# Kernel tuning notes

Hardware: AMD Instinct MI355X
Metric: run time of the kernel (lower is better)

## Reference

```python
import jax, jax.numpy as jnp
import numpy as np

DIM = 1024
NUM_HEADS = 16
NUM_KV_HEADS = 4
HEAD_DIM = DIM // NUM_HEADS  # 64
GROUP = NUM_HEADS // NUM_KV_HEADS  # 4
SCALE = HEAD_DIM ** -0.5


def setup_inputs() -> dict:
    key = jax.random.key(0)
    ks = jax.random.split(key, 6)
    B, N = 2, 2048
    x = jax.random.normal(ks[0], (B, N, DIM), dtype=jnp.float32)
    s = DIM ** -0.5
    Wq = jax.random.normal(ks[1], (DIM, DIM), dtype=jnp.float32) * s
    Wk = jax.random.normal(ks[2], (DIM, NUM_KV_HEADS * HEAD_DIM), dtype=jnp.float32) * s
    Wv = jax.random.normal(ks[3], (DIM, NUM_KV_HEADS * HEAD_DIM), dtype=jnp.float32) * s
    Wo = jax.random.normal(ks[4], (DIM, DIM), dtype=jnp.float32) * s
    bo = jax.random.normal(ks[5], (DIM,), dtype=jnp.float32) * 0.01
    return {"x": x, "Wq": Wq, "Wk": Wk, "Wv": Wv, "Wo": Wo, "bo": bo}


def reference(x, Wq, Wk, Wv, Wo, bo):
    B, N, C = x.shape
    # projections
    q = (x @ Wq).reshape(B, N, NUM_HEADS, HEAD_DIM)          # B N H D
    k = (x @ Wk).reshape(B, N, NUM_KV_HEADS, HEAD_DIM)       # B N Kh D
    v = (x @ Wv).reshape(B, N, NUM_KV_HEADS, HEAD_DIM)
    # group query heads: H = Kh * GROUP; broadcast KV per group (no repeat copy)
    q = q.reshape(B, N, NUM_KV_HEADS, GROUP, HEAD_DIM)
    # scores: B Kh G Nq Nk
    attn = jnp.einsum('bqhgd,bkhd->bhgqk', q, k) * SCALE
    attn = jax.nn.softmax(attn, axis=-1)
    out = jnp.einsum('bhgqk,bkhd->bqhgd', attn, v)           # B N Kh G D
    out = out.reshape(B, N, C)
    return out @ Wo + bo
```

## Files before the change

### kernel.cpp

```cpp
#include <hip/hip_runtime.h>
#include <hip/hip_bf16.h>


typedef unsigned short u16;
typedef short s8 __attribute__((ext_vector_type(8)));
typedef short s4 __attribute__((ext_vector_type(4)));
typedef float f4 __attribute__((ext_vector_type(4)));
typedef u16 u16x8 __attribute__((ext_vector_type(8)));
typedef unsigned int u32x4 __attribute__((ext_vector_type(4)));

__device__ __forceinline__ unsigned pk2(float a, float b) {
  __hip_bfloat162 h = __float22bfloat162_rn(make_float2(a, b));
  unsigned u; __builtin_memcpy(&u, &h, 4); return u;
}
__device__ __forceinline__ u16 bf1(float a) {
  __hip_bfloat16 h = __float2bfloat16(a);
  u16 u; __builtin_memcpy(&u, &h, 2); return u;
}
__device__ __forceinline__ float ex2(float x) { return exp2f(x); }
__device__ __forceinline__ void glds16(const u16* g, u16* l) {
  __builtin_amdgcn_global_load_lds((const __attribute__((address_space(1))) unsigned*)g,
                                   (__attribute__((address_space(3))) unsigned*)l, 16, 0, 0);
}

__global__ __launch_bounds__(256) void cvt_all(const float* __restrict__ x,
                                               const float* __restrict__ Wq, const float* __restrict__ Wk,
                                               const float* __restrict__ Wv, const float* __restrict__ Wo,
                                               u16* __restrict__ xb, u16* __restrict__ wqkvt,
                                               u16* __restrict__ wot) {
  if (blockIdx.z == 4) {
    const int base = (blockIdx.y * 16 + blockIdx.x) * 256 + threadIdx.x;
#pragma unroll
    for (int j = 0; j < 16; ++j) {
      const int i = base + j * 65536;
      float4 f = ((const float4*)x)[i];
      uint2 o; o.x = pk2(f.x, f.y); o.y = pk2(f.z, f.w);
      ((uint2*)xb)[i] = o;
    }
    return;
  }
  __shared__ u16 T[64][68];
  const int m = blockIdx.z;
  const float* src; u16* dst; int N; int drow0; float scale;
  if (m == 0)      { src = Wq; N = 1024; dst = wqkvt; drow0 = 0;    scale = 0.18033688011112042f; }
  else if (m == 1) { src = Wk; N = 256;  dst = wqkvt; drow0 = 1024; scale = 1.f; }
  else if (m == 2) { src = Wv; N = 256;  dst = wqkvt; drow0 = 1280; scale = 1.f; }
  else             { src = Wo; N = 1024; dst = wot;   drow0 = 0;    scale = 1.f; }
  const int n0 = blockIdx.x * 64, k0 = blockIdx.y * 64;
  if (n0 >= N) return;
  const int tid = threadIdx.x;
  const int rr = tid >> 4, cc = (tid & 15) * 4;
#pragma unroll
  for (int it = 0; it < 4; ++it) {
    const int r = rr + it * 16;
    float4 f = *(const float4*)&src[(k0 + r) * N + n0 + cc];
    uint2 o; o.x = pk2(f.x * scale, f.y * scale); o.y = pk2(f.z * scale, f.w * scale);
    *(uint2*)&T[r][cc] = o;
  }
  __syncthreads();
  const int nn = tid >> 3, kq = (tid & 7) * 8;
#pragma unroll
  for (int it = 0; it < 2; ++it) {
    const int n = nn + it * 32;
    u16x8 v;
#pragma unroll
    for (int j = 0; j < 8; ++j) v[j] = T[kq + j][n];
    *(u16x8*)&dst[(drow0 + n0 + n) * 1024 + k0 + kq] = v;
  }
}

__global__ __launch_bounds__(256) void vtrans(const u16* __restrict__ vc, u16* __restrict__ vt) {
  __shared__ u16 T[64][72];
  const int tok0 = blockIdx.x * 64, d0 = blockIdx.y * 64, b = blockIdx.z;
  const int tid = threadIdx.x;
  const int r = tid >> 3, cc = (tid & 7) * 8;
#pragma unroll
  for (int it = 0; it < 2; ++it) {
    const int row = r + it * 32;
    *(u16x8*)&T[row][cc] = *(const u16x8*)&vc[(b * 2048 + tok0 + row) * 256 + d0 + cc];
  }
  __syncthreads();
#pragma unroll
  for (int it = 0; it < 2; ++it) {
    const int d = (tid >> 3) + it * 32;
    const int gd = d0 + d, kh = gd >> 6, dd = gd & 63;
    u16x8 v;
#pragma unroll
    for (int j = 0; j < 8; ++j) v[j] = T[(tid & 7) * 8 + j][d];
    *(u16x8*)&vt[((b * 4 + kh) * 64 + dd) * 2048 + tok0 + (tid & 7) * 8] = v;
  }
}

template<int MODE>
__global__ __launch_bounds__(256) void gemm_bt(const u16* __restrict__ A, const u16* __restrict__ Bt,
                                               u16* __restrict__ Cq, u16* __restrict__ Vc,
                                               float* __restrict__ Cf, const float* __restrict__ bias,
                                               const int K) {
  __shared__ u16 As[64 * 32];
  __shared__ u16 Bs[128 * 32];
  const int tid = threadIdx.x, lane = tid & 63, w = tid >> 6;
  const int wm = w >> 1, wn = w & 1;
  const int m0 = blockIdx.y * 64, n0 = blockIdx.x * 128;
  const int g = lane >> 4, c = lane & 15;
  const int l2 = lane >> 2, ch = (lane & 3) * 8;
  const u16* ga = A + (m0 + w * 16 + l2) * K + ch;
  const u16* gb = Bt + (n0 + w * 32 + l2) * K + ch;
  f4 acc[2][4] = {};
  for (int k0 = 0; k0 < K; k0 += 32) {
    glds16(ga,           &As[w * 512]);
    glds16(gb,           &Bs[w * 1024]);
    glds16(gb + 16 * K,  &Bs[w * 1024 + 512]);
    ga += 32; gb += 32;
    __syncthreads();
    s8 a[2], b2[4];
#pragma unroll
    for (int m = 0; m < 2; ++m) a[m] = *(const s8*)&As[(wm * 32 + m * 16 + c) * 32 + g * 8];
#pragma unroll
    for (int n = 0; n < 4; ++n) b2[n] = *(const s8*)&Bs[(wn * 64 + n * 16 + c) * 32 + g * 8];
    __builtin_amdgcn_s_setprio(1);
#pragma unroll
    for (int m = 0; m < 2; ++m)
#pragma unroll
      for (int n = 0; n < 4; ++n)
        acc[m][n] = __builtin_amdgcn_mfma_f32_16x16x32_bf16(a[m], b2[n], acc[m][n], 0, 0, 0);
    __builtin_amdgcn_s_setprio(0);
    __syncthreads();
  }
#pragma unroll
  for (int m = 0; m < 2; ++m) {
#pragma unroll
    for (int n = 0; n < 4; ++n) {
#pragma unroll
      for (int r = 0; r < 4; ++r) {
        const int row = m0 + wm * 32 + m * 16 + g * 4 + r;
        const int col = n0 + wn * 64 + n * 16 + c;
        if (MODE == 0) {
          const u16 hv = bf1(acc[m][n][r]);
          if (col < 1280) Cq[row * 1280 + col] = hv;
          else            Vc[row * 256 + (col - 1280)] = hv;
        } else {
          Cf[row * 1024 + col] = acc[m][n][r] + bias[col];
        }
      }
    }
  }
}

__global__ __launch_bounds__(256, 2) void attn_fwd(const u16* __restrict__ qkv,
                                                   const u16* __restrict__ vt,
                                                   u16* __restrict__ ao) {
  __shared__ u16 SMEM[32768];
  const int tid = threadIdx.x, lane = tid & 63, w = tid >> 6;
  const int h = blockIdx.y, b = blockIdx.z, kh = h >> 2;
  const int q0 = blockIdx.x * 64;
  const int g = lane >> 4, c = lane & 15;
  const int l3 = lane >> 3, ch8 = lane & 7;
  const int l4 = lane >> 4, ch16 = lane & 15;

  const u16* kgb = qkv + (b * 2048) * 1280 + 1024 + kh * 64;
  const u16* vgb = vt + ((b * 4 + kh) * 64) * 2048;

  s8 qf[4][2];
#pragma unroll
  for (int qb = 0; qb < 4; ++qb) {
    const u16* qr = qkv + (b * 2048 + q0 + qb * 16 + c) * 1280 + h * 64;
    qf[qb][0] = *(const s8*)&qr[g * 8];
    qf[qb][1] = *(const s8*)&qr[32 + g * 8];
  }

  auto stageKV = [&](int it, int bo) {
#pragma unroll
    for (int i = 0; i < 4; ++i) {
      const int kr = w * 32 + i * 8 + l3;
      glds16(kgb + (it * 128 + kr) * 1280 + ((ch8 ^ (kr & 7)) << 3),
             &SMEM[bo + (w * 32 + i * 8) * 64]);
    }
#pragma unroll
    for (int i = 0; i < 4; ++i) {
      const int vd = w * 16 + i * 4 + l4;
      glds16(vgb + vd * 2048 + it * 128 + ((ch16 ^ (vd & 7)) << 3),
             &SMEM[16384 + bo + (w * 16 + i * 4) * 128]);
    }
  };

  stageKV(0, 0);
  __syncthreads();

  s8 ones;
#pragma unroll
  for (int j = 0; j < 8; ++j) ones[j] = (short)0x3F80;

  f4 acc[4][4] = {};
  f4 accS[4] = {};
  int bo = 0;

  for (int it = 0; it < 16; ++it) {
    if (it < 15) stageKV(it + 1, bo ^ 8192);

    s8 kf[2][2];
#pragma unroll
    for (int mf = 0; mf < 2; ++mf) {
      const int krow = bo + (w * 32 + mf * 16 + c) * 64;
      kf[mf][0] = *(const s8*)&SMEM[krow + ((g ^ (c & 7)) << 3)];
      kf[mf][1] = *(const s8*)&SMEM[krow + (((4 + g) ^ (c & 7)) << 3)];
    }
    s8 vf[4];
#pragma unroll
    for (int df = 0; df < 4; ++df) {
      const int drow = 16384 + bo + (df * 16 + c) * 128;
      const int cw = c & 7;
      s4 v0 = *(const s4*)&SMEM[drow + (((w * 4 + (g >> 1)) ^ cw) << 3) + (g & 1) * 4];
      s4 v1 = *(const s4*)&SMEM[drow + (((w * 4 + 2 + (g >> 1)) ^ cw) << 3) + (g & 1) * 4];
      vf[df] = __builtin_shufflevector(v0, v1, 0, 1, 2, 3, 4, 5, 6, 7);
    }

    __builtin_amdgcn_s_setprio(1);
#pragma unroll
    for (int qb = 0; qb < 4; ++qb) {
      f4 s0 = {}, s1 = {};
      s0 = __builtin_amdgcn_mfma_f32_16x16x32_bf16(kf[0][0], qf[qb][0], s0, 0, 0, 0);
      s0 = __builtin_amdgcn_mfma_f32_16x16x32_bf16(kf[0][1], qf[qb][1], s0, 0, 0, 0);
      s1 = __builtin_amdgcn_mfma_f32_16x16x32_bf16(kf[1][0], qf[qb][0], s1, 0, 0, 0);
      s1 = __builtin_amdgcn_mfma_f32_16x16x32_bf16(kf[1][1], qf[qb][1], s1, 0, 0, 0);
      u32x4 pw;
      pw.x = pk2(ex2(s0[0]), ex2(s0[1]));
      pw.y = pk2(ex2(s0[2]), ex2(s0[3]));
      pw.z = pk2(ex2(s1[0]), ex2(s1[1]));
      pw.w = pk2(ex2(s1[2]), ex2(s1[3]));
      s8 pb; __builtin_memcpy(&pb, &pw, 16);
      accS[qb] = __builtin_amdgcn_mfma_f32_16x16x32_bf16(ones, pb, accS[qb], 0, 0, 0);
#pragma unroll
      for (int df = 0; df < 4; ++df)
        acc[df][qb] = __builtin_amdgcn_mfma_f32_16x16x32_bf16(vf[df], pb, acc[df][qb], 0, 0, 0);
    }
    __builtin_amdgcn_s_setprio(0);
    __syncthreads();
    bo ^= 8192;
  }

  float* red = (float*)SMEM;
#pragma unroll
  for (int df = 0; df < 4; ++df)
#pragma unroll
    for (int qb = 0; qb < 4; ++qb)
      *(f4*)&red[(w * 16 + df * 4 + qb) * 256 + lane * 4] = acc[df][qb];
  __syncthreads();
  f4 sum[4];
#pragma unroll
  for (int qb = 0; qb < 4; ++qb) {
    f4 t = {};
#pragma unroll
    for (int j = 0; j < 4; ++j)
      t += *(const f4*)&red[(j * 16 + w * 4 + qb) * 256 + lane * 4];
    sum[qb] = t;
  }
  __syncthreads();
  float* sden = (float*)SMEM;
#pragma unroll
  for (int qb = 0; qb < 4; ++qb) sden[(w * 4 + qb) * 64 + lane] = accS[qb][0];
  __syncthreads();
#pragma unroll
  for (int qb = 0; qb < 4; ++qb) {
    float den = 0.f;
#pragma unroll
    for (int j = 0; j < 4; ++j) den += sden[(j * 4 + qb) * 64 + lane];
    const float inv = 1.f / den;
    uint2 o;
    o.x = pk2(sum[qb][0] * inv, sum[qb][1] * inv);
    o.y = pk2(sum[qb][2] * inv, sum[qb][3] * inv);
    *(uint2*)&ao[(b * 2048 + q0 + qb * 16 + c) * 1024 + h * 64 + w * 16 + g * 4] = o;
  }
}

extern "C" void kernel_launch(void* const* d_in, const int* in_sizes, int n_in,
                              void* d_out, int out_size, void* d_ws, size_t ws_size,
                              hipStream_t stream) {
  const float* x  = (const float*)d_in[0];
  const float* Wq = (const float*)d_in[1];
  const float* Wk = (const float*)d_in[2];
  const float* Wv = (const float*)d_in[3];
  const float* Wo = (const float*)d_in[4];
  const float* bo = (const float*)d_in[5];
  float* out = (float*)d_out;

  char* ws = (char*)d_ws;
  u16* xb    = (u16*)(ws);
  u16* ao    = (u16*)(ws);
  u16* wqkvt = (u16*)(ws + 8388608);
  u16* wot   = (u16*)(ws + 11534336);
  u16* qkv   = (u16*)(ws + 13631488);
  u16* vtw   = (u16*)(ws + 24117248);
  u16* vc    = (u16*)(ws + 26214400);

  cvt_all<<<dim3(16, 16, 5), 256, 0, stream>>>(x, Wq, Wk, Wv, Wo, xb, wqkvt, wot);
  gemm_bt<0><<<dim3(12, 64), 256, 0, stream>>>(xb, wqkvt, qkv, vc, nullptr, nullptr, 1024);
  vtrans<<<dim3(32, 4, 2), 256, 0, stream>>>(vc, vtw);
  attn_fwd<<<dim3(32, 16, 2), 256, 0, stream>>>(qkv, vtw, ao);
  gemm_bt<1><<<dim3(8, 64), 256, 0, stream>>>(ao, wot, nullptr, nullptr, out, bo, 1024);
}
```

Before: 193.5 us.

## Double-buffer GEMM LDS tiles and shrink attention tiles for higher occupancy

The projection GEMM now prefetches the next K-slice into a second LDS buffer while computing on the current one, so global-to-LDS loads overlap with MFMA work. The attention kernel halves its query tile to 32 and its KV tile to 64, cuts LDS use, and raises launch bounds to 4 blocks per SM with twice as many blocks. Only half of each P operand is filled (the upper half is zero), which wastes half of the PV and row-sum MFMA throughput in exchange for more occupancy and less LDS pressure.

New measurement: 201.3 us. 1.04x slower.

```diff
diff --git a/kernel.cpp b/kernel.cpp
--- a/kernel.cpp
+++ b/kernel.cpp
@@ -96,8 +96,7 @@
                                                u16* __restrict__ Cq, u16* __restrict__ Vc,
                                                float* __restrict__ Cf, const float* __restrict__ bias,
                                                const int K) {
-  __shared__ u16 As[64 * 32];
-  __shared__ u16 Bs[128 * 32];
+  __shared__ u16 S[12288];
   const int tid = threadIdx.x, lane = tid & 63, w = tid >> 6;
   const int wm = w >> 1, wn = w & 1;
   const int m0 = blockIdx.y * 64, n0 = blockIdx.x * 128;
@@ -106,17 +105,26 @@
   const u16* ga = A + (m0 + w * 16 + l2) * K + ch;
   const u16* gb = Bt + (n0 + w * 32 + l2) * K + ch;
   f4 acc[2][4] = {};
-  for (int k0 = 0; k0 < K; k0 += 32) {
-    glds16(ga,           &As[w * 512]);
-    glds16(gb,           &Bs[w * 1024]);
-    glds16(gb + 16 * K,  &Bs[w * 1024 + 512]);
-    ga += 32; gb += 32;
-    __syncthreads();
+  const int nk = K >> 5;
+  glds16(ga,          &S[w * 512]);
+  glds16(gb,          &S[4096 + w * 1024]);
+  glds16(gb + 16 * K, &S[4096 + w * 1024 + 512]);
+  __syncthreads();
+  int buf = 0;
+  for (int k0 = 0; k0 < nk; ++k0) {
+    if (k0 + 1 < nk) {
+      ga += 32; gb += 32;
+      const int ab = (buf ^ 1) * 2048, bb = 4096 + (buf ^ 1) * 4096;
+      glds16(ga,          &S[ab + w * 512]);
+      glds16(gb,          &S[bb + w * 1024]);
+      glds16(gb + 16 * K, &S[bb + w * 1024 + 512]);
+    }
+    const int ab = buf * 2048, bb = 4096 + buf * 4096;
     s8 a[2], b2[4];
 #pragma unroll
-    for (int m = 0; m < 2; ++m) a[m] = *(const s8*)&As[(wm * 32 + m * 16 + c) * 32 + g * 8];
-#pragma unroll
-    for (int n = 0; n < 4; ++n) b2[n] = *(const s8*)&Bs[(wn * 64 + n * 16 + c) * 32 + g * 8];
+    for (int m = 0; m < 2; ++m) a[m] = *(const s8*)&S[ab + (wm * 32 + m * 16 + c) * 32 + g * 8];
+#pragma unroll
+    for (int n = 0; n < 4; ++n) b2[n] = *(const s8*)&S[bb + (wn * 64 + n * 16 + c) * 32 + g * 8];
     __builtin_amdgcn_s_setprio(1);
 #pragma unroll
     for (int m = 0; m < 2; ++m)
@@ -125,6 +133,7 @@
         acc[m][n] = __builtin_amdgcn_mfma_f32_16x16x32_bf16(a[m], b2[n], acc[m][n], 0, 0, 0);
     __builtin_amdgcn_s_setprio(0);
     __syncthreads();
+    buf ^= 1;
   }
 #pragma unroll
   for (int m = 0; m < 2; ++m) {
@@ -146,87 +155,73 @@
   }
 }
 
-__global__ __launch_bounds__(256, 2) void attn_fwd(const u16* __restrict__ qkv,
+__global__ __launch_bounds__(256, 4) void attn_fwd(const u16* __restrict__ qkv,
                                                    const u16* __restrict__ vt,
                                                    u16* __restrict__ ao) {
-  __shared__ u16 SMEM[32768];
+  __shared__ u16 SMEM[16384];
   const int tid = threadIdx.x, lane = tid & 63, w = tid >> 6;
   const int h = blockIdx.y, b = blockIdx.z, kh = h >> 2;
-  const int q0 = blockIdx.x * 64;
+  const int q0 = blockIdx.x * 32;
   const int g = lane >> 4, c = lane & 15;
   const int l3 = lane >> 3, ch8 = lane & 7;
-  const int l4 = lane >> 4, ch16 = lane & 15;
-
-  const u16* kgb = qkv + (b * 2048) * 1280 + 1024 + kh * 64;
-  const u16* vgb = vt + ((b * 4 + kh) * 64) * 2048;
-
-  s8 qf[4][2];
-#pragma unroll
-  for (int qb = 0; qb < 4; ++qb) {
+
+  s8 qf[2][2];
+#pragma unroll
+  for (int qb = 0; qb < 2; ++qb) {
     const u16* qr = qkv + (b * 2048 + q0 + qb * 16 + c) * 1280 + h * 64;
     qf[qb][0] = *(const s8*)&qr[g * 8];
     qf[qb][1] = *(const s8*)&qr[32 + g * 8];
   }
 
-  auto stageKV = [&](int it, int bo) {
-#pragma unroll
-    for (int i = 0; i < 4; ++i) {
-      const int kr = w * 32 + i * 8 + l3;
-      glds16(kgb + (it * 128 + kr) * 1280 + ((ch8 ^ (kr & 7)) << 3),
-             &SMEM[bo + (w * 32 + i * 8) * 64]);
-    }
-#pragma unroll
-    for (int i = 0; i < 4; ++i) {
-      const int vd = w * 16 + i * 4 + l4;
-      glds16(vgb + vd * 2048 + it * 128 + ((ch16 ^ (vd & 7)) << 3),
-             &SMEM[16384 + bo + (w * 16 + i * 4) * 128]);
-    }
-  };
-
-  stageKV(0, 0);
-  __syncthreads();
-
+  const int swz = (ch8 ^ l3) << 3;
+  const u16* kg0 = qkv + (b * 2048 + w * 16 + l3) * 1280 + 1024 + kh * 64 + swz;
+  const u16* kg1 = kg0 + 8 * 1280;
+  const u16* vg0 = vt + ((b * 4 + kh) * 64 + w * 16 + l3) * 2048 + swz;
+  const u16* vg1 = vg0 + 8 * 2048;
+  const int kd0 = (w * 16) * 64, kd1 = (w * 16 + 8) * 64;
+
+  glds16(kg0, &SMEM[kd0]);        glds16(kg1, &SMEM[kd1]);
+  glds16(vg0, &SMEM[8192 + kd0]); glds16(vg1, &SMEM[8192 + kd1]);
+  __syncthreads();
+
+  const int cw = c & 7;
+  const int kb0 = (w * 16 + c) * 64 + ((g ^ cw) << 3);
+  const int kb1 = (w * 16 + c) * 64 + (((4 + g) ^ cw) << 3);
+  const int vch = ((w * 2 + (g >> 1)) ^ cw) * 8 + (g & 1) * 4;
+
+  f4 acc[4][2] = {};
+  f4 accS[2] = {};
   s8 ones;
 #pragma unroll
   for (int j = 0; j < 8; ++j) ones[j] = (short)0x3F80;
-
-  f4 acc[4][4] = {};
-  f4 accS[4] = {};
   int bo = 0;
 
-  for (int it = 0; it < 16; ++it) {
-    if (it < 15) stageKV(it + 1, bo ^ 8192);
-
-    s8 kf[2][2];
-#pragma unroll
-    for (int mf = 0; mf < 2; ++mf) {
-      const int krow = bo + (w * 32 + mf * 16 + c) * 64;
-      kf[mf][0] = *(const s8*)&SMEM[krow + ((g ^ (c & 7)) << 3)];
-      kf[mf][1] = *(const s8*)&SMEM[krow + (((4 + g) ^ (c & 7)) << 3)];
-    }
+  for (int it = 0; it < 32; ++it) {
+    if (it < 31) {
+      kg0 += 64 * 1280; kg1 += 64 * 1280; vg0 += 64; vg1 += 64;
+      const int nb = bo ^ 4096;
+      glds16(kg0, &SMEM[nb + kd0]);        glds16(kg1, &SMEM[nb + kd1]);
+      glds16(vg0, &SMEM[8192 + nb + kd0]); glds16(vg1, &SMEM[8192 + nb + kd1]);
+    }
+    const s8 kf0 = *(const s8*)&SMEM[bo + kb0];
+    const s8 kf1 = *(const s8*)&SMEM[bo + kb1];
     s8 vf[4];
 #pragma unroll
     for (int df = 0; df < 4; ++df) {
-      const int drow = 16384 + bo + (df * 16 + c) * 128;
-      const int cw = c & 7;
-      s4 v0 = *(const s4*)&SMEM[drow + (((w * 4 + (g >> 1)) ^ cw) << 3) + (g & 1) * 4];
-      s4 v1 = *(const s4*)&SMEM[drow + (((w * 4 + 2 + (g >> 1)) ^ cw) << 3) + (g & 1) * 4];
-      vf[df] = __builtin_shufflevector(v0, v1, 0, 1, 2, 3, 4, 5, 6, 7);
+      const s4 v0 = *(const s4*)&SMEM[8192 + bo + (df * 16 + c) * 64 + vch];
+      vf[df] = __builtin_shufflevector(v0, v0, 0, 1, 2, 3, 0, 1, 2, 3);
     }
 
     __builtin_amdgcn_s_setprio(1);
 #pragma unroll
-    for (int qb = 0; qb < 4; ++qb) {
-      f4 s0 = {}, s1 = {};
-      s0 = __builtin_amdgcn_mfma_f32_16x16x32_bf16(kf[0][0], qf[qb][0], s0, 0, 0, 0);
-      s0 = __builtin_amdgcn_mfma_f32_16x16x32_bf16(kf[0][1], qf[qb][1], s0, 0, 0, 0);
-      s1 = __builtin_amdgcn_mfma_f32_16x16x32_bf16(kf[1][0], qf[qb][0], s1, 0, 0, 0);
-      s1 = __builtin_amdgcn_mfma_f32_16x16x32_bf16(kf[1][1], qf[qb][1], s1, 0, 0, 0);
+    for (int qb = 0; qb < 2; ++qb) {
+      f4 s0 = {};
+      s0 = __builtin_amdgcn_mfma_f32_16x16x32_bf16(kf0, qf[qb][0], s0, 0, 0, 0);
+      s0 = __builtin_amdgcn_mfma_f32_16x16x32_bf16(kf1, qf[qb][1], s0, 0, 0, 0);
       u32x4 pw;
       pw.x = pk2(ex2(s0[0]), ex2(s0[1]));
       pw.y = pk2(ex2(s0[2]), ex2(s0[3]));
-      pw.z = pk2(ex2(s1[0]), ex2(s1[1]));
-      pw.w = pk2(ex2(s1[2]), ex2(s1[3]));
+      pw.z = 0u; pw.w = 0u;
       s8 pb; __builtin_memcpy(&pb, &pw, 16);
       accS[qb] = __builtin_amdgcn_mfma_f32_16x16x32_bf16(ones, pb, accS[qb], 0, 0, 0);
 #pragma unroll
@@ -235,35 +230,35 @@
     }
     __builtin_amdgcn_s_setprio(0);
     __syncthreads();
-    bo ^= 8192;
+    bo ^= 4096;
   }
 
   float* red = (float*)SMEM;
 #pragma unroll
   for (int df = 0; df < 4; ++df)
 #pragma unroll
-    for (int qb = 0; qb < 4; ++qb)
-      *(f4*)&red[(w * 16 + df * 4 + qb) * 256 + lane * 4] = acc[df][qb];
-  __syncthreads();
-  f4 sum[4];
-#pragma unroll
-  for (int qb = 0; qb < 4; ++qb) {
+    for (int qb = 0; qb < 2; ++qb)
+      *(f4*)&red[(w * 8 + df * 2 + qb) * 256 + lane * 4] = acc[df][qb];
+  __syncthreads();
+  f4 sum[2];
+#pragma unroll
+  for (int qb = 0; qb < 2; ++qb) {
     f4 t = {};
 #pragma unroll
     for (int j = 0; j < 4; ++j)
-      t += *(const f4*)&red[(j * 16 + w * 4 + qb) * 256 + lane * 4];
+      t += *(const f4*)&red[(j * 8 + w * 2 + qb) * 256 + lane * 4];
     sum[qb] = t;
   }
   __syncthreads();
   float* sden = (float*)SMEM;
 #pragma unroll
-  for (int qb = 0; qb < 4; ++qb) sden[(w * 4 + qb) * 64 + lane] = accS[qb][0];
-  __syncthreads();
-#pragma unroll
-  for (int qb = 0; qb < 4; ++qb) {
+  for (int qb = 0; qb < 2; ++qb) sden[(w * 2 + qb) * 64 + lane] = accS[qb][0];
+  __syncthreads();
+#pragma unroll
+  for (int qb = 0; qb < 2; ++qb) {
     float den = 0.f;
 #pragma unroll
-    for (int j = 0; j < 4; ++j) den += sden[(j * 4 + qb) * 64 + lane];
+    for (int j = 0; j < 4; ++j) den += sden[(j * 2 + qb) * 64 + lane];
     const float inv = 1.f / den;
     uint2 o;
     o.x = pk2(sum[qb][0] * inv, sum[qb][1] * inv);
@@ -295,6 +290,6 @@
   cvt_all<<<dim3(16, 16, 5), 256, 0, stream>>>(x, Wq, Wk, Wv, Wo, xb, wqkvt, wot);
   gemm_bt<0><<<dim3(12, 64), 256, 0, stream>>>(xb, wqkvt, qkv, vc, nullptr, nullptr, 1024);
   vtrans<<<dim3(32, 4, 2), 256, 0, stream>>>(vc, vtw);
-  attn_fwd<<<dim3(32, 16, 2), 256, 0, stream>>>(qkv, vtw, ao);
+  attn_fwd<<<dim3(64, 16, 2), 256, 0, stream>>>(qkv, vtw, ao);
   gemm_bt<1><<<dim3(8, 64), 256, 0, stream>>>(ao, wot, nullptr, nullptr, out, bo, 1024);
 }
```
